# Kernel optimization log

Measured on AMD Instinct MI355X. Metric: run time of the kernel, lower is better.

The kernel has to match this reference:

```python
import jax, jax.numpy as jnp
import numpy as np

BATCH_SIZE = 4096
TEMPERATURE = 0.5
DIAG_NEG = -50000.0
EPS = 1e-8  # torch CosineSimilarity eps


def setup_inputs() -> dict:
    key = jax.random.key(0)
    k1, k2 = jax.random.split(key)
    z_i = jax.random.normal(k1, (BATCH_SIZE, 128), dtype=jnp.float32)
    z_j = jax.random.normal(k2, (BATCH_SIZE, 128), dtype=jnp.float32)
    return {"z_i": z_i, "z_j": z_j}


def reference(z_i, z_j):
    n = z_i.shape[0]
    z = jnp.concatenate([z_i, z_j], axis=0)  # [2N, D]
    # cosine similarity: normalize once, then one GEMM (same math as
    # CosineSimilarity(dim=2) on the broadcasted pair, with eps clamp on norms)
    norms = jnp.maximum(jnp.linalg.norm(z, axis=-1, keepdims=True), EPS)
    zn = z / norms
    sim = (zn @ zn.T) / TEMPERATURE  # [2N, 2N]
    # mask self-similarity on the diagonal
    idx = jnp.arange(2 * n)
    sim = sim.at[idx, idx].set(DIAG_NEG)
    # labels: positive pair is the other view
    labels = jnp.concatenate([idx[n:], idx[:n]])  # [2N]
    # mean softmax cross-entropy
    logp = jax.nn.log_softmax(sim, axis=-1)
    loss = -jnp.mean(logp[idx, labels])
    return loss
```

## Files before the change

kernel.cpp:

```cpp
#include <hip/hip_runtime.h>

#define N2 8192
#define NHALF 4096
#define DDIM 128
#define NCHUNK 16
#define CPC 512
#define NT 8
#define LN2F 0.69314718055994530942f
#define SCALEF 1.6986436f

typedef __attribute__((ext_vector_type(8))) short bf8_t;
typedef __attribute__((ext_vector_type(4))) float f4_t;

__device__ __forceinline__ float fexp2(float x) { return __builtin_amdgcn_exp2f(x); }
__device__ __forceinline__ float flog2(float x) { return __builtin_amdgcn_logf(x); }

__device__ __forceinline__ unsigned short f2bf(float f) {
  unsigned int x = __float_as_uint(f);
  x += 0x7fffu + ((x >> 16) & 1u);
  return (unsigned short)(x >> 16);
}
__device__ __forceinline__ float bf2f(unsigned short h) {
  return __uint_as_float(((unsigned int)h) << 16);
}

__global__ __launch_bounds__(256) void knorm(const float* __restrict__ zi,
                                             const float* __restrict__ zj,
                                             unsigned short* __restrict__ u,
                                             float* __restrict__ dhat) {
  const int lane = threadIdx.x & 63;
  const int row = blockIdx.x * 4 + (threadIdx.x >> 6);
  const float* src = (row < NHALF) ? (zi + (size_t)row * DDIM)
                                   : (zj + (size_t)(row - NHALF) * DDIM);
  float2 x = *(const float2*)(src + lane * 2);
  float ss = x.x * x.x + x.y * x.y;
#pragma unroll
  for (int m = 32; m; m >>= 1) ss += __shfl_xor(ss, m);
  float scale = SCALEF / fmaxf(sqrtf(ss), 1e-8f);
  unsigned short b0 = f2bf(x.x * scale);
  unsigned short b1 = f2bf(x.y * scale);
  *(unsigned int*)(u + (size_t)row * DDIM + lane * 2) =
      (unsigned int)b0 | ((unsigned int)b1 << 16);
  float f0 = bf2f(b0), f1 = bf2f(b1);
  float dd = f0 * f0 + f1 * f1;
#pragma unroll
  for (int m = 32; m; m >>= 1) dd += __shfl_xor(dd, m);
  if (lane == 0) dhat[row] = dd;
}

__global__ __launch_bounds__(512) void ksim(const unsigned short* __restrict__ u,
                                            float* __restrict__ Lp) {
  __shared__ short Bls[32768];
  const int tid = threadIdx.x;
  const int lane = tid & 63;
  const int w = tid >> 6;
  const int rb = blockIdx.x >> 4;
  const int chunk = blockIdx.x & 15;
  const int lr = lane & 15, lq = lane >> 4;
  const int rowbase = rb * 256 + w * 32;
  const int colbase = chunk * CPC;

  bf8_t a[2][4];
#pragma unroll
  for (int s = 0; s < 2; s++)
#pragma unroll
    for (int kc = 0; kc < 4; kc++)
      a[s][kc] = *(const bf8_t*)(u + (size_t)(rowbase + s * 16 + lr) * DDIM +
                                 kc * 32 + lq * 8);
#pragma unroll
  for (int s = 0; s < 2; s++)
#pragma unroll
    for (int kc = 0; kc < 4; kc++)
      asm volatile("" : "+v"(a[s][kc]));

  f4_t L0 = {0.f, 0.f, 0.f, 0.f}, L1 = {0.f, 0.f, 0.f, 0.f};

  auto STAGE = [&](int t) {
#pragma unroll
    for (int i = 0; i < 2; i++) {
      const int j = w * 2 + i;
      const int col_local = j * 4 + lq;
      const int sdu = lr ^ (4 * (j & 1) + lq);
      const unsigned short* src =
          u + (size_t)(colbase + t * 64 + col_local) * DDIM + sdu * 8;
      short* dst = &Bls[(t & 3) * 8192 + j * 512];
      __builtin_amdgcn_global_load_lds(
          (const __attribute__((address_space(1))) unsigned int*)src,
          (__attribute__((address_space(3))) unsigned int*)dst, 16, 0, 0);
    }
  };

  auto COMP = [&](int t) {
    const short* P = &Bls[(t & 3) * 8192];
#pragma unroll
    for (int g = 0; g < 4; g++) {
      bf8_t bv[4];
#pragma unroll
      for (int kc = 0; kc < 4; kc++)
        bv[kc] = *(const bf8_t*)&P[((g * 16 + lr) * 16 +
                                    ((kc * 4 + lq) ^ (lr & 7))) * 8];
      f4_t acc0 = {0.f, 0.f, 0.f, 0.f}, acc1 = {0.f, 0.f, 0.f, 0.f};
#pragma unroll
      for (int kc = 0; kc < 4; kc++) {
        acc0 = __builtin_amdgcn_mfma_f32_16x16x32_bf16(a[0][kc], bv[kc], acc0, 0, 0, 0);
        acc1 = __builtin_amdgcn_mfma_f32_16x16x32_bf16(a[1][kc], bv[kc], acc1, 0, 0, 0);
      }
#pragma unroll
      for (int r = 0; r < 4; r++) {
        L0[r] += fexp2(acc0[r]);
        L1[r] += fexp2(acc1[r]);
      }
    }
  };

  STAGE(0); STAGE(1); STAGE(2); STAGE(3);
#pragma unroll 1
  for (int t = 0; t < NT; t += 2) {
    if (t < NT - 2) {
      asm volatile("s_waitcnt vmcnt(4)" ::: "memory");
    } else {
      asm volatile("s_waitcnt vmcnt(0)" ::: "memory");
    }
    __builtin_amdgcn_sched_barrier(0);
    __builtin_amdgcn_s_barrier();
    __builtin_amdgcn_sched_barrier(0);
    COMP(t);
    COMP(t + 1);
    if (t + 2 < NT) STAGE(t + 2);
    if (t + 3 < NT) STAGE(t + 3);
  }

#pragma unroll
  for (int r = 0; r < 4; r++) {
    float v0 = L0[r], v1 = L1[r];
    v0 += __shfl_xor(v0, 1); v0 += __shfl_xor(v0, 2);
    v0 += __shfl_xor(v0, 4); v0 += __shfl_xor(v0, 8);
    v1 += __shfl_xor(v1, 1); v1 += __shfl_xor(v1, 2);
    v1 += __shfl_xor(v1, 4); v1 += __shfl_xor(v1, 8);
    if (lr == 0) {
      const int rrow = rowbase + lq * 4 + r;
      Lp[(size_t)rrow * NCHUNK + chunk] = v0;
      Lp[(size_t)(rrow + 16) * NCHUNK + chunk] = v1;
    }
  }
}

__global__ __launch_bounds__(256) void krow(const unsigned short* __restrict__ u,
                                            const float* __restrict__ dhat,
                                            const float* __restrict__ Lp,
                                            float* __restrict__ bsum) {
  const int lane = threadIdx.x & 63;
  const int w = threadIdx.x >> 6;
  const int i = blockIdx.x * 4 + w;
  const int j = (i + NHALF) & (N2 - 1);

  const unsigned int av = ((const unsigned int*)(u + (size_t)i * DDIM))[lane];
  const unsigned int bv = ((const unsigned int*)(u + (size_t)j * DDIM))[lane];
  float dot = __uint_as_float(av << 16) * __uint_as_float(bv << 16) +
              __uint_as_float(av & 0xffff0000u) * __uint_as_float(bv & 0xffff0000u);
  float ls = (lane < NCHUNK) ? Lp[(size_t)i * NCHUNK + lane] : 0.f;
#pragma unroll
  for (int m = 32; m; m >>= 1) {
    dot += __shfl_xor(dot, m);
    ls += __shfl_xor(ls, m);
  }
  __shared__ float sred[4];
  if (lane == 0) {
    const float L = ls - fexp2(dhat[i]);
    sred[w] = LN2F * (flog2(L) - dot);
  }
  __syncthreads();
  if (threadIdx.x == 0)
    bsum[blockIdx.x] = sred[0] + sred[1] + sred[2] + sred[3];
}

__global__ void kfinal(const float* __restrict__ bsum, float* __restrict__ out) {
  float v = 0.f;
#pragma unroll
  for (int jj = 0; jj < 32; jj++) v += bsum[threadIdx.x + 64 * jj];
#pragma unroll
  for (int m = 32; m; m >>= 1) v += __shfl_xor(v, m);
  if (threadIdx.x == 0) out[0] = v * (1.0f / N2);
}

extern "C" void kernel_launch(void* const* d_in, const int* in_sizes, int n_in,
                              void* d_out, int out_size, void* d_ws, size_t ws_size,
                              hipStream_t stream) {
  const float* zi = (const float*)d_in[0];
  const float* zj = (const float*)d_in[1];
  char* ws = (char*)d_ws;
  unsigned short* u = (unsigned short*)ws;
  float* dhat = (float*)(ws + (size_t)N2 * DDIM * 2);
  float* Lp = (float*)(ws + (size_t)N2 * DDIM * 2 + (size_t)N2 * 4);
  float* bsum = (float*)(ws + (size_t)N2 * DDIM * 2 + (size_t)N2 * 4 +
                         (size_t)NCHUNK * N2 * 4);
  float* out = (float*)d_out;

  hipLaunchKernelGGL(knorm, dim3(N2 / 4), dim3(256), 0, stream, zi, zj, u, dhat);
  hipLaunchKernelGGL(ksim, dim3((N2 / 256) * NCHUNK), dim3(512), 0, stream, u, Lp);
  hipLaunchKernelGGL(krow, dim3(N2 / 4), dim3(256), 0, stream, u, dhat, Lp, bsum);
  hipLaunchKernelGGL(kfinal, dim3(1), dim3(64), 0, stream, bsum, out);
}
```

Baseline: 37.75 us.

## Stage A tiles via LDS, triple-buffer B pipeline, fuse final reduction via atomics

```diff
diff --git a/kernel.cpp b/kernel.cpp
--- a/kernel.cpp
+++ b/kernel.cpp
@@ -8,6 +8,7 @@
 #define NT 8
 #define LN2F 0.69314718055994530942f
 #define SCALEF 1.6986436f
+#define FXSCALE 1073741824.0
 
 typedef __attribute__((ext_vector_type(8))) short bf8_t;
 typedef __attribute__((ext_vector_type(4))) float f4_t;
@@ -27,7 +28,10 @@
 __global__ __launch_bounds__(256) void knorm(const float* __restrict__ zi,
                                              const float* __restrict__ zj,
                                              unsigned short* __restrict__ u,
-                                             float* __restrict__ dhat) {
+                                             float* __restrict__ dhat,
+                                             unsigned long long* __restrict__ acc,
+                                             unsigned int* __restrict__ ticket) {
+  if (blockIdx.x == 0 && threadIdx.x == 0) { acc[0] = 0ull; ticket[0] = 0u; }
   const int lane = threadIdx.x & 63;
   const int row = blockIdx.x * 4 + (threadIdx.x >> 6);
   const float* src = (row < NHALF) ? (zi + (size_t)row * DDIM)
@@ -57,21 +61,42 @@
   const int rb = blockIdx.x >> 4;
   const int chunk = blockIdx.x & 15;
   const int lr = lane & 15, lq = lane >> 4;
-  const int rowbase = rb * 256 + w * 32;
+  const int rowbase = rb * 256;
   const int colbase = chunk * CPC;
 
+#pragma unroll
+  for (int i = 0; i < 8; i++) {
+    const int k = w * 8 + i;
+    const int row_local = k * 4 + lq;
+    const int sdu = lr ^ (4 * (k & 1) + lq);
+    const unsigned short* src =
+        u + (size_t)(rowbase + row_local) * DDIM + sdu * 8;
+    short* dst = &Bls[k * 512];
+    __builtin_amdgcn_global_load_lds(
+        (const __attribute__((address_space(1))) unsigned int*)src,
+        (__attribute__((address_space(3))) unsigned int*)dst, 16, 0, 0);
+  }
+  asm volatile("s_waitcnt vmcnt(0)" ::: "memory");
+  __builtin_amdgcn_sched_barrier(0);
+  __builtin_amdgcn_s_barrier();
+  __builtin_amdgcn_sched_barrier(0);
+
   bf8_t a[2][4];
 #pragma unroll
   for (int s = 0; s < 2; s++)
 #pragma unroll
-    for (int kc = 0; kc < 4; kc++)
-      a[s][kc] = *(const bf8_t*)(u + (size_t)(rowbase + s * 16 + lr) * DDIM +
-                                 kc * 32 + lq * 8);
+    for (int kc = 0; kc < 4; kc++) {
+      const int R = w * 32 + s * 16 + lr;
+      a[s][kc] = *(const bf8_t*)&Bls[(R * 16 + ((kc * 4 + lq) ^ (lr & 7))) * 8];
+    }
 #pragma unroll
   for (int s = 0; s < 2; s++)
 #pragma unroll
     for (int kc = 0; kc < 4; kc++)
       asm volatile("" : "+v"(a[s][kc]));
+  __builtin_amdgcn_sched_barrier(0);
+  __builtin_amdgcn_s_barrier();
+  __builtin_amdgcn_sched_barrier(0);
 
   f4_t L0 = {0.f, 0.f, 0.f, 0.f}, L1 = {0.f, 0.f, 0.f, 0.f};
 
@@ -83,7 +108,7 @@
       const int sdu = lr ^ (4 * (j & 1) + lq);
       const unsigned short* src =
           u + (size_t)(colbase + t * 64 + col_local) * DDIM + sdu * 8;
-      short* dst = &Bls[(t & 3) * 8192 + j * 512];
+      short* dst = &Bls[(t % 3) * 8192 + j * 512];
       __builtin_amdgcn_global_load_lds(
           (const __attribute__((address_space(1))) unsigned int*)src,
           (__attribute__((address_space(3))) unsigned int*)dst, 16, 0, 0);
@@ -91,7 +116,7 @@
   };
 
   auto COMP = [&](int t) {
-    const short* P = &Bls[(t & 3) * 8192];
+    const short* P = &Bls[(t % 3) * 8192];
 #pragma unroll
     for (int g = 0; g < 4; g++) {
       bf8_t bv[4];
@@ -113,11 +138,12 @@
     }
   };
 
-  STAGE(0); STAGE(1); STAGE(2); STAGE(3);
+  STAGE(0);
+  STAGE(1);
 #pragma unroll 1
-  for (int t = 0; t < NT; t += 2) {
-    if (t < NT - 2) {
-      asm volatile("s_waitcnt vmcnt(4)" ::: "memory");
+  for (int t = 0; t < NT; ++t) {
+    if (t < NT - 1) {
+      asm volatile("s_waitcnt vmcnt(2)" ::: "memory");
     } else {
       asm volatile("s_waitcnt vmcnt(0)" ::: "memory");
     }
@@ -125,9 +151,7 @@
     __builtin_amdgcn_s_barrier();
     __builtin_amdgcn_sched_barrier(0);
     COMP(t);
-    COMP(t + 1);
     if (t + 2 < NT) STAGE(t + 2);
-    if (t + 3 < NT) STAGE(t + 3);
   }
 
 #pragma unroll
@@ -138,7 +162,7 @@
     v1 += __shfl_xor(v1, 1); v1 += __shfl_xor(v1, 2);
     v1 += __shfl_xor(v1, 4); v1 += __shfl_xor(v1, 8);
     if (lr == 0) {
-      const int rrow = rowbase + lq * 4 + r;
+      const int rrow = rowbase + w * 32 + lq * 4 + r;
       Lp[(size_t)rrow * NCHUNK + chunk] = v0;
       Lp[(size_t)(rrow + 16) * NCHUNK + chunk] = v1;
     }
@@ -148,7 +172,9 @@
 __global__ __launch_bounds__(256) void krow(const unsigned short* __restrict__ u,
                                             const float* __restrict__ dhat,
                                             const float* __restrict__ Lp,
-                                            float* __restrict__ bsum) {
+                                            unsigned long long* __restrict__ acc,
+                                            unsigned int* __restrict__ ticket,
+                                            float* __restrict__ out) {
   const int lane = threadIdx.x & 63;
   const int w = threadIdx.x >> 6;
   const int i = blockIdx.x * 4 + w;
@@ -170,17 +196,18 @@
     sred[w] = LN2F * (flog2(L) - dot);
   }
   __syncthreads();
-  if (threadIdx.x == 0)
-    bsum[blockIdx.x] = sred[0] + sred[1] + sred[2] + sred[3];
-}
-
-__global__ void kfinal(const float* __restrict__ bsum, float* __restrict__ out) {
-  float v = 0.f;
-#pragma unroll
-  for (int jj = 0; jj < 32; jj++) v += bsum[threadIdx.x + 64 * jj];
-#pragma unroll
-  for (int m = 32; m; m >>= 1) v += __shfl_xor(v, m);
-  if (threadIdx.x == 0) out[0] = v * (1.0f / N2);
+  if (threadIdx.x == 0) {
+    const float part = sred[0] + sred[1] + sred[2] + sred[3];
+    const unsigned long long q =
+        (unsigned long long)((double)part * FXSCALE + 0.5);
+    atomicAdd(acc, q);
+    __threadfence();
+    const unsigned int old = atomicAdd(ticket, 1u);
+    if (old == (unsigned int)(N2 / 4 - 1)) {
+      const unsigned long long tot = atomicAdd(acc, 0ull);
+      out[0] = (float)((double)tot * (1.0 / FXSCALE) * (1.0 / N2));
+    }
+  }
 }
 
 extern "C" void kernel_launch(void* const* d_in, const int* in_sizes, int n_in,
@@ -192,12 +219,15 @@
   unsigned short* u = (unsigned short*)ws;
   float* dhat = (float*)(ws + (size_t)N2 * DDIM * 2);
   float* Lp = (float*)(ws + (size_t)N2 * DDIM * 2 + (size_t)N2 * 4);
-  float* bsum = (float*)(ws + (size_t)N2 * DDIM * 2 + (size_t)N2 * 4 +
-                         (size_t)NCHUNK * N2 * 4);
+  unsigned long long* acc =
+      (unsigned long long*)(ws + (size_t)N2 * DDIM * 2 + (size_t)N2 * 4 +
+                            (size_t)NCHUNK * N2 * 4);
+  unsigned int* ticket = (unsigned int*)(acc + 1);
   float* out = (float*)d_out;
 
-  hipLaunchKernelGGL(knorm, dim3(N2 / 4), dim3(256), 0, stream, zi, zj, u, dhat);
+  hipLaunchKernelGGL(knorm, dim3(N2 / 4), dim3(256), 0, stream, zi, zj, u, dhat,
+                     acc, ticket);
   hipLaunchKernelGGL(ksim, dim3((N2 / 256) * NCHUNK), dim3(512), 0, stream, u, Lp);
-  hipLaunchKernelGGL(krow, dim3(N2 / 4), dim3(256), 0, stream, u, dhat, Lp, bsum);
-  hipLaunchKernelGGL(kfinal, dim3(1), dim3(64), 0, stream, bsum, out);
-}
+  hipLaunchKernelGGL(krow, dim3(N2 / 4), dim3(256), 0, stream, u, dhat, Lp,
+                     acc, ticket, out);
+}
```

New measurement: 82.45 us. +118.4%, slower.
